# Performance work log

Hardware: AMD Instinct MI355X
Metric: run time of the kernel (lower is better)

## Reference

```python
import jax, jax.numpy as jnp
import numpy as np

B, D, K = 16384, 256, 1024

def setup_inputs() -> dict:
    key = jax.random.key(0)
    k1, k2 = jax.random.split(key)
    x = jax.random.normal(k1, (B, D), dtype=jnp.float32)
    centers = jax.random.uniform(k2, (K, D), dtype=jnp.float32)  # RandomUniform(0,1)
    betas = jnp.ones((K,), dtype=jnp.float32)
    return {"x": x, "centers": centers, "betas": betas}

def reference(x, centers, betas):
    x_sq = jnp.sum(x * x, axis=-1, keepdims=True)          # [B,1]
    c_sq = jnp.sum(centers * centers, axis=-1)             # [K]
    cross = jnp.einsum('bd,kd->bk', x, centers)            # [B,K]
    diffnorm = x_sq + c_sq[None, :] - 2.0 * cross          # [B,K]
    return jnp.exp(-betas[None, :] * diffnorm)             # [B,K]
```

## Files before the change

kernel.cpp:

```cpp
#include <hip/hip_runtime.h>
#include <stdint.h>

#define D_DIM 256
#define K_CTR 1024
#define B_ROWS 16384
#define BM 32

typedef float f32x4 __attribute__((ext_vector_type(4)));
typedef float f32x2 __attribute__((ext_vector_type(2)));
typedef long long i64x2 __attribute__((ext_vector_type(2)));

static __device__ __forceinline__ unsigned cvt4_fp8(const float4 v) {
    int r = __builtin_amdgcn_cvt_pk_fp8_f32(v.x, v.y, 0, false);
    r = __builtin_amdgcn_cvt_pk_fp8_f32(v.z, v.w, r, true);
    return (unsigned)r;
}

static __device__ __forceinline__ void barrier_lgkm() {
    asm volatile("s_waitcnt lgkmcnt(0)" ::: "memory");
    __builtin_amdgcn_s_barrier();
}

__global__ __launch_bounds__(256) void rbf_prep(const float* __restrict__ centers,
                                                unsigned char* __restrict__ cbf,
                                                float* __restrict__ csq) {
    const int w = threadIdx.x >> 6;
    const int l = threadIdx.x & 63;
    const int c0 = blockIdx.x * 4 + w;
    const float4 v = *reinterpret_cast<const float4*>(centers + c0 * D_DIM + l * 4);
    float s = v.x * v.x + v.y * v.y + v.z * v.z + v.w * v.w;
    const unsigned u = cvt4_fp8(v);
    const unsigned off = (unsigned)((c0 >> 4) * 4096 + (l >> 4) * 1024
                       + (((l >> 1) & 3) * 16 + (c0 & 15)) * 16
                       + ((l >> 3) & 1) * 8 + (l & 1) * 4);
    *reinterpret_cast<unsigned*>(cbf + off) = u;
    #pragma unroll
    for (int off2 = 1; off2 < 64; off2 <<= 1) s += __shfl_xor(s, off2);
    if (l == 0) csq[c0] = s;
}

__global__ __launch_bounds__(512, 4) void rbf_main(const float* __restrict__ x,
                                                   const unsigned char* __restrict__ cbf,
                                                   const float* __restrict__ csq,
                                                   const float* __restrict__ betas,
                                                   float* __restrict__ out) {
    __shared__ __align__(16) unsigned char As[BM * D_DIM];
    __shared__ __align__(16) float obuf[2][BM * 128];
    __shared__ float xs_lds[BM];

    const int tid = threadIdx.x;
    const int w = tid >> 6;
    const int l = tid & 63;
    const int strip = (blockIdx.x & 7) * 64 + (blockIdx.x >> 3);
    const int row0 = strip * BM;

    #pragma unroll
    for (int i = 0; i < 4; ++i) {
        const int r = i * 8 + w;
        const float4 v = *reinterpret_cast<const float4*>(x + (size_t)(row0 + r) * D_DIM + l * 4);
        float s = v.x * v.x + v.y * v.y + v.z * v.z + v.w * v.w;
        const unsigned u = cvt4_fp8(v);
        const unsigned pos = (unsigned)((l >> 4) * 64 + ((l >> 1) & 3) * 16
                           + ((l >> 3) & 1) * 8 + (l & 1) * 4);
        *reinterpret_cast<unsigned*>(As + r * 256 + (pos ^ ((unsigned)(r & 7) << 4))) = u;
        #pragma unroll
        for (int off = 1; off < 64; off <<= 1) s += __shfl_xor(s, off);
        if (l == 0) xs_lds[r] = s;
    }

    const int hk = l >> 4;
    const int lr = l & 15;
    const unsigned char* bwave = cbf + l * 16;

    i64x2 b0[4], b1[4];
    {
        const unsigned char* bbase = bwave + w * 4096;
        #pragma unroll
        for (int p = 0; p < 4; ++p)
            b0[p] = *reinterpret_cast<const i64x2*>(bbase + p * 1024);
    }
    barrier_lgkm();

    i64x2 a[2][4];
    #pragma unroll
    for (int m = 0; m < 2; ++m) {
        const int r = m * 16 + lr;
        #pragma unroll
        for (int p = 0; p < 4; ++p)
            a[m][p] = *reinterpret_cast<const i64x2*>(
                As + r * 256 + ((unsigned)(p * 64 + hk * 16) ^ ((unsigned)(lr & 7) << 4)));
    }
    const float xs0 = xs_lds[lr];
    const float xs1 = xs_lds[16 + lr];
    const float LOG2E = 1.4426950408889634f;

    #pragma unroll
    for (int ph = 0; ph < 8; ++ph) {
        const int colp = ph * 128;
        const i64x2 (&bc)[4] = (ph & 1) ? b1 : b0;
        i64x2 (&bn)[4] = (ph & 1) ? b0 : b1;

        if (ph < 7) {
            const unsigned char* bbase = bwave + ((ph + 1) * 8 + w) * 4096;
            #pragma unroll
            for (int p = 0; p < 4; ++p)
                bn[p] = *reinterpret_cast<const i64x2*>(bbase + p * 1024);
        }

        f32x4 acc[2] = {};
        #pragma unroll
        for (int p = 0; p < 4; ++p)
            #pragma unroll
            for (int m = 0; m < 2; ++m) {
                acc[m] = __builtin_amdgcn_mfma_f32_16x16x32_fp8_fp8(bc[p][0], a[m][p][0], acc[m], 0, 0, 0);
                acc[m] = __builtin_amdgcn_mfma_f32_16x16x32_fp8_fp8(bc[p][1], a[m][p][1], acc[m], 0, 0, 0);
            }

        float* ob = obuf[ph & 1];
        {
            const int cl = w * 16 + hk * 4;
            const f32x4 cs = *reinterpret_cast<const f32x4*>(csq + colp + cl);
            const f32x4 bt = *reinterpret_cast<const f32x4*>(betas + colp + cl);
            f32x4 btl2, coef2, base;
            #pragma unroll
            for (int j = 0; j < 4; ++j) {
                btl2[j] = bt[j] * LOG2E;
                coef2[j] = btl2[j] + btl2[j];
                base[j] = -btl2[j] * cs[j];
            }
            #pragma unroll
            for (int m = 0; m < 2; ++m) {
                const int r = m * 16 + lr;
                const float xsv = m ? xs1 : xs0;
                f32x4 rv;
                #pragma unroll
                for (int j = 0; j < 4; ++j) {
                    const float c0 = __builtin_fmaf(-btl2[j], xsv, base[j]);
                    rv[j] = __builtin_exp2f(__builtin_fmaf(coef2[j], acc[m][j], c0));
                }
                *reinterpret_cast<f32x4*>(reinterpret_cast<char*>(ob)
                    + r * 512 + ((unsigned)(cl * 4) ^ ((unsigned)(r & 7) << 4))) = rv;
            }
        }
        barrier_lgkm();

        #pragma unroll
        for (int i = 0; i < 4; ++i) {
            const int r = w * 4 + i;
            const f32x2 v = *reinterpret_cast<const f32x2*>(reinterpret_cast<const char*>(obuf[ph & 1])
                    + r * 512 + ((unsigned)(l * 8) ^ ((unsigned)(r & 7) << 4)));
            *reinterpret_cast<f32x2*>(out + (size_t)(row0 + r) * K_CTR + colp + l * 2) = v;
        }
    }
}

extern "C" void kernel_launch(void* const* d_in, const int* in_sizes, int n_in,
                              void* d_out, int out_size, void* d_ws, size_t ws_size,
                              hipStream_t stream) {
    const float* x       = (const float*)d_in[0];
    const float* centers = (const float*)d_in[1];
    const float* betas   = (const float*)d_in[2];
    float* out = (float*)d_out;

    unsigned char* cbf = (unsigned char*)d_ws;
    float* csq = (float*)((char*)d_ws + (size_t)K_CTR * D_DIM);

    rbf_prep<<<K_CTR / 4, 256, 0, stream>>>(centers, cbf, csq);
    rbf_main<<<B_ROWS / BM, 512, 0, stream>>>(x, cbf, csq, betas, out);
}
```

Before: 27.33 us.

## Move x fp8 conversion and row norms into prep kernel, stage stores

Quantization of x to fp8 and the row squared norms now run in the prep kernel, which writes a pre-swizzled fp8 buffer to workspace. The main kernel then only copies 8KB per strip into LDS instead of reading 32KB of fp32 and doing shuffle reductions. The epilogue math is simplified, and the LDS reads for the output are batched ahead of the global stores with a double-buffered register set. The cost is an extra workspace round trip for x and a larger prep launch, traded for less prologue latency in the main kernel.

```diff
diff --git a/kernel.cpp b/kernel.cpp
--- a/kernel.cpp
+++ b/kernel.cpp
@@ -5,10 +5,12 @@
 #define K_CTR 1024
 #define B_ROWS 16384
 #define BM 32
+#define NSTRIP (B_ROWS / BM)
 
 typedef float f32x4 __attribute__((ext_vector_type(4)));
 typedef float f32x2 __attribute__((ext_vector_type(2)));
 typedef long long i64x2 __attribute__((ext_vector_type(2)));
+typedef unsigned int u32x4 __attribute__((ext_vector_type(4)));
 
 static __device__ __forceinline__ unsigned cvt4_fp8(const float4 v) {
     int r = __builtin_amdgcn_cvt_pk_fp8_f32(v.x, v.y, 0, false);
@@ -21,32 +23,55 @@
     __builtin_amdgcn_s_barrier();
 }
 
-__global__ __launch_bounds__(256) void rbf_prep(const float* __restrict__ centers,
+static __device__ __forceinline__ unsigned lane_pos(int l) {
+    return (unsigned)((l >> 4) * 64 + ((l >> 1) & 3) * 16 + ((l >> 3) & 1) * 8 + (l & 1) * 4);
+}
+
+__global__ __launch_bounds__(256) void rbf_prep(const float* __restrict__ x,
+                                                const float* __restrict__ centers,
                                                 unsigned char* __restrict__ cbf,
-                                                float* __restrict__ csq) {
+                                                float* __restrict__ csq,
+                                                unsigned char* __restrict__ xb,
+                                                float* __restrict__ xsq) {
     const int w = threadIdx.x >> 6;
     const int l = threadIdx.x & 63;
-    const int c0 = blockIdx.x * 4 + w;
-    const float4 v = *reinterpret_cast<const float4*>(centers + c0 * D_DIM + l * 4);
-    float s = v.x * v.x + v.y * v.y + v.z * v.z + v.w * v.w;
-    const unsigned u = cvt4_fp8(v);
-    const unsigned off = (unsigned)((c0 >> 4) * 4096 + (l >> 4) * 1024
-                       + (((l >> 1) & 3) * 16 + (c0 & 15)) * 16
-                       + ((l >> 3) & 1) * 8 + (l & 1) * 4);
-    *reinterpret_cast<unsigned*>(cbf + off) = u;
-    #pragma unroll
-    for (int off2 = 1; off2 < 64; off2 <<= 1) s += __shfl_xor(s, off2);
-    if (l == 0) csq[c0] = s;
+    if (blockIdx.x < 2048) {
+        #pragma unroll
+        for (int i = 0; i < 2; ++i) {
+            const int row = blockIdx.x * 8 + i * 4 + w;
+            const float4 v = *reinterpret_cast<const float4*>(x + (size_t)row * D_DIM + l * 4);
+            float s = v.x * v.x + v.y * v.y + v.z * v.z + v.w * v.w;
+            const unsigned u = cvt4_fp8(v);
+            const int strip = row >> 5, rloc = row & 31;
+            *reinterpret_cast<unsigned*>(xb + (size_t)strip * 8192 + rloc * 256
+                + (lane_pos(l) ^ ((unsigned)(rloc & 7) << 4))) = u;
+            #pragma unroll
+            for (int off = 1; off < 64; off <<= 1) s += __shfl_xor(s, off);
+            if (l == 0) xsq[row] = s;
+        }
+    } else {
+        const int c0 = (blockIdx.x - 2048) * 4 + w;
+        const float4 v = *reinterpret_cast<const float4*>(centers + c0 * D_DIM + l * 4);
+        float s = v.x * v.x + v.y * v.y + v.z * v.z + v.w * v.w;
+        const unsigned u = cvt4_fp8(v);
+        const unsigned off = (unsigned)((c0 >> 4) * 4096 + (l >> 4) * 1024
+                           + (((l >> 1) & 3) * 16 + (c0 & 15)) * 16
+                           + ((l >> 3) & 1) * 8 + (l & 1) * 4);
+        *reinterpret_cast<unsigned*>(cbf + off) = u;
+        #pragma unroll
+        for (int off2 = 1; off2 < 64; off2 <<= 1) s += __shfl_xor(s, off2);
+        if (l == 0) csq[c0] = s;
+    }
 }
 
-__global__ __launch_bounds__(512, 4) void rbf_main(const float* __restrict__ x,
+__global__ __launch_bounds__(512, 4) void rbf_main(const unsigned char* __restrict__ xb,
+                                                   const float* __restrict__ xsq,
                                                    const unsigned char* __restrict__ cbf,
                                                    const float* __restrict__ csq,
                                                    const float* __restrict__ betas,
                                                    float* __restrict__ out) {
     __shared__ __align__(16) unsigned char As[BM * D_DIM];
     __shared__ __align__(16) float obuf[2][BM * 128];
-    __shared__ float xs_lds[BM];
 
     const int tid = threadIdx.x;
     const int w = tid >> 6;
@@ -54,18 +79,9 @@
     const int strip = (blockIdx.x & 7) * 64 + (blockIdx.x >> 3);
     const int row0 = strip * BM;
 
-    #pragma unroll
-    for (int i = 0; i < 4; ++i) {
-        const int r = i * 8 + w;
-        const float4 v = *reinterpret_cast<const float4*>(x + (size_t)(row0 + r) * D_DIM + l * 4);
-        float s = v.x * v.x + v.y * v.y + v.z * v.z + v.w * v.w;
-        const unsigned u = cvt4_fp8(v);
-        const unsigned pos = (unsigned)((l >> 4) * 64 + ((l >> 1) & 3) * 16
-                           + ((l >> 3) & 1) * 8 + (l & 1) * 4);
-        *reinterpret_cast<unsigned*>(As + r * 256 + (pos ^ ((unsigned)(r & 7) << 4))) = u;
-        #pragma unroll
-        for (int off = 1; off < 64; off <<= 1) s += __shfl_xor(s, off);
-        if (l == 0) xs_lds[r] = s;
+    {
+        const u32x4 v = *reinterpret_cast<const u32x4*>(xb + (size_t)strip * 8192 + tid * 16);
+        *reinterpret_cast<u32x4*>(As + tid * 16) = v;
     }
 
     const int hk = l >> 4;
@@ -90,9 +106,11 @@
             a[m][p] = *reinterpret_cast<const i64x2*>(
                 As + r * 256 + ((unsigned)(p * 64 + hk * 16) ^ ((unsigned)(lr & 7) << 4)));
     }
-    const float xs0 = xs_lds[lr];
-    const float xs1 = xs_lds[16 + lr];
+    const float xs0 = xsq[row0 + lr];
+    const float xs1 = xsq[row0 + 16 + lr];
     const float LOG2E = 1.4426950408889634f;
+
+    f32x2 svA[4] = {}, svB[4] = {};
 
     #pragma unroll
     for (int ph = 0; ph < 8; ++ph) {
@@ -121,13 +139,6 @@
             const int cl = w * 16 + hk * 4;
             const f32x4 cs = *reinterpret_cast<const f32x4*>(csq + colp + cl);
             const f32x4 bt = *reinterpret_cast<const f32x4*>(betas + colp + cl);
-            f32x4 btl2, coef2, base;
-            #pragma unroll
-            for (int j = 0; j < 4; ++j) {
-                btl2[j] = bt[j] * LOG2E;
-                coef2[j] = btl2[j] + btl2[j];
-                base[j] = -btl2[j] * cs[j];
-            }
             #pragma unroll
             for (int m = 0; m < 2; ++m) {
                 const int r = m * 16 + lr;
@@ -135,8 +146,9 @@
                 f32x4 rv;
                 #pragma unroll
                 for (int j = 0; j < 4; ++j) {
-                    const float c0 = __builtin_fmaf(-btl2[j], xsv, base[j]);
-                    rv[j] = __builtin_exp2f(__builtin_fmaf(coef2[j], acc[m][j], c0));
+                    const float btl2 = bt[j] * LOG2E;
+                    const float cc = -btl2 * (xsv + cs[j]);
+                    rv[j] = __builtin_exp2f(__builtin_fmaf(btl2 + btl2, acc[m][j], cc));
                 }
                 *reinterpret_cast<f32x4*>(reinterpret_cast<char*>(ob)
                     + r * 512 + ((unsigned)(cl * 4) ^ ((unsigned)(r & 7) << 4))) = rv;
@@ -144,12 +156,19 @@
         }
         barrier_lgkm();
 
+        f32x2 (&sv)[4]  = (ph & 1) ? svB : svA;
+        f32x2 (&svo)[4] = (ph & 1) ? svA : svB;
+        asm volatile("" :: "v"(svo[0]), "v"(svo[1]), "v"(svo[2]), "v"(svo[3]));
         #pragma unroll
         for (int i = 0; i < 4; ++i) {
             const int r = w * 4 + i;
-            const f32x2 v = *reinterpret_cast<const f32x2*>(reinterpret_cast<const char*>(obuf[ph & 1])
+            sv[i] = *reinterpret_cast<const f32x2*>(reinterpret_cast<const char*>(obuf[ph & 1])
                     + r * 512 + ((unsigned)(l * 8) ^ ((unsigned)(r & 7) << 4)));
-            *reinterpret_cast<f32x2*>(out + (size_t)(row0 + r) * K_CTR + colp + l * 2) = v;
+        }
+        #pragma unroll
+        for (int i = 0; i < 4; ++i) {
+            const int r = w * 4 + i;
+            *reinterpret_cast<f32x2*>(out + (size_t)(row0 + r) * K_CTR + colp + l * 2) = sv[i];
         }
     }
 }
@@ -163,8 +182,10 @@
     float* out = (float*)d_out;
 
     unsigned char* cbf = (unsigned char*)d_ws;
-    float* csq = (float*)((char*)d_ws + (size_t)K_CTR * D_DIM);
+    float* csq = (float*)((char*)d_ws + 262144);
+    unsigned char* xb  = (unsigned char*)d_ws + 262144 + 4096;
+    float* xsq = (float*)((char*)d_ws + 262144 + 4096 + (size_t)NSTRIP * 8192);
 
-    rbf_prep<<<K_CTR / 4, 256, 0, stream>>>(centers, cbf, csq);
-    rbf_main<<<B_ROWS / BM, 512, 0, stream>>>(x, cbf, csq, betas, out);
+    rbf_prep<<<2048 + K_CTR / 4, 256, 0, stream>>>(x, centers, cbf, csq, xb, xsq);
+    rbf_main<<<NSTRIP, 512, 0, stream>>>(xb, xsq, cbf, csq, betas, out);
 }
```

New measurement: 26.55 us, median of 2. 2.8% less time.
